# Performance work log

Hardware: AMD Instinct MI355X
Metric: run time of the kernel (lower is better)

## Reference

```python
import jax, jax.numpy as jnp
import numpy as np
from jax import lax

# pywt Wavelet('db3') analysis filters (dec_lo, dec_hi)
DEC_LO = jnp.array([0.035226291882100656, -0.08544127388224149, -0.13501102001039084,
                    0.4598775021193313, 0.8068915093133388, 0.3326705529509569], dtype=jnp.float32)
DEC_HI = jnp.array([-0.3326705529509569, 0.8068915093133388, -0.4598775021193313,
                    -0.13501102001039084, 0.08544127388224149, 0.035226291882100656], dtype=jnp.float32)


def _dwt_level(x):
    # One analysis level of pytorch_wavelets DWT1D with mode='zero'.
    # x: [B, N] -> (lo, hi) each [B, (N+L-1)//2]
    N = x.shape[-1]
    L = DEC_LO.shape[0]
    outsize = (N + L - 1) // 2  # pywt.dwt_coeff_len, zero mode
    p = 2 * (outsize - 1) - N + L
    # conv_general_dilated does cross-correlation; reversed filter == true convolution
    w = jnp.stack([DEC_LO[::-1], DEC_HI[::-1]])[:, None, :]  # [2, 1, L]
    y = lax.conv_general_dilated(x[:, None, :], w, window_strides=(2,),
                                 padding=[(p // 2, p - p // 2)])  # [B, 2, outsize]
    return y[:, 0, :], y[:, 1, :]


def _wavelet_features(sig, level=3):
    # sig: [B, N]. Returns (mean of final low-pass, sum over levels of ||hf||_2) per row.
    lo = sig
    high = jnp.zeros(sig.shape[0], sig.dtype)
    for _ in range(level):
        lo, hi = _dwt_level(lo)
        high = high + jnp.sqrt(jnp.sum(hi * hi, axis=-1))
    return jnp.mean(lo, axis=-1), high


def _dirichlet_weight(low, high):
    # Deterministic surrogate: Dirichlet([a1*10, a2*10]) has mean a1/(a1+a2),
    # replacing scipy dirichlet.rvs sampling with its expectation.
    a1 = jnp.clip(low, 1e-6)
    a2 = jnp.clip(high, 1e-6)
    return a1 / (a1 + a2)


def _forward(user_idx, item_idx, values, num_users, num_items):
    # item popularity: scatter-add of values * log1p(interaction count), L2-normalized
    counts = jnp.zeros(num_items, jnp.float32).at[item_idx].add(1.0)
    log_counts = jnp.log1p(counts)
    pop = jnp.zeros(num_items, jnp.float32).at[item_idx].add(values * log_counts[item_idx])
    pop = pop / (jnp.linalg.norm(pop) + 1e-8)
    # user activity
    act = jnp.zeros(num_users, jnp.float32).at[user_idx].add(
        values / jnp.log1p(pop[item_idx] + 1e-8))
    act = act / (jnp.linalg.norm(act) + 1e-8)
    # dense per-entity interaction signals (batched scatter replaces per-entity masking loop)
    user_sig = jnp.zeros((num_users, num_items), jnp.float32).at[user_idx, item_idx].add(values)
    user_sig = user_sig * (1.0 + act)[:, None]
    item_sig = jnp.zeros((num_items, num_users), jnp.float32).at[item_idx, user_idx].add(values)
    item_sig = item_sig * (1.0 + pop)[:, None]
    u_low, u_high = _wavelet_features(user_sig)
    i_low, i_high = _wavelet_features(item_sig)
    u_pop = _dirichlet_weight(u_low, u_high)
    i_pop = _dirichlet_weight(i_low, i_high)
    u_ni, i_ni = 1.0 - u_pop, 1.0 - i_pop
    wu_p, wu_n = u_pop[user_idx], u_ni[user_idx]
    wi_p, wi_n = i_pop[item_idx], i_ni[item_idx]
    # nnz-valued sparse outputs: [UIPG(=pop/pop), UING(=niche/niche), pop/niche, niche/pop]
    return jnp.stack([values * wu_p * wi_p,
                      values * wu_n * wi_n,
                      values * wu_p * wi_n,
                      values * wu_n * wi_p])


def setup_inputs():
    key = jax.random.key(0)
    k1, k2, k3 = jax.random.split(key, 3)
    NNZ, U, I = 2_000_000, 8192, 8192
    return {
        "user_idx": jax.random.randint(k1, (NNZ,), 0, U, dtype=jnp.int32),
        "item_idx": jax.random.randint(k2, (NNZ,), 0, I, dtype=jnp.int32),
        "values": jax.random.uniform(k3, (NNZ,), dtype=jnp.float32),
        "num_users": U,
        "num_items": I,
    }


def reference(user_idx, item_idx, values, num_users, num_items):
    return _forward(user_idx, item_idx, values, num_users, num_items)
```

## Files before the change

### kernel.cpp

```cpp
#include <hip/hip_runtime.h>
#include <math.h>

#define NE 8192
#define HT 1024
#define NCH 8
#define RT 512
#define NROWS 16

__device__ __constant__ float LO_R[6] = {
    0.3326705529509569f, 0.8068915093133388f, 0.4598775021193313f,
    -0.13501102001039084f, -0.08544127388224149f, 0.035226291882100656f};
__device__ __constant__ float HI_RV[6] = {
    0.035226291882100656f, 0.08544127388224149f, -0.13501102001039084f,
    -0.4598775021193313f, 0.8068915093133388f, -0.3326705529509569f};

__device__ __forceinline__ float blockReduceSum(float v, float* red) {
    #pragma unroll
    for (int off = 32; off > 0; off >>= 1) v += __shfl_down(v, off);
    int lane = threadIdx.x & 63, wid = threadIdx.x >> 6;
    if (lane == 0) red[wid] = v;
    __syncthreads();
    float r = 0.f;
    if (threadIdx.x == 0) {
        int nw = blockDim.x >> 6;
        for (int i = 0; i < nw; ++i) r += red[i];
    }
    return r;
}

__global__ void k_tables(float* __restrict__ resp, float4* __restrict__ Tdiag) {
    int a = blockIdx.x * blockDim.x + threadIdx.x;
    if (a >= NE) return;
    float lo1r[8], hi1r[8];
    int k1a = max(0, (a >> 1) - 3);
    #pragma unroll
    for (int t = 0; t < 8; ++t) {
        int k = k1a + t;
        int j = a - 2 * k + 4;
        bool ok = (j >= 0 && j <= 5 && k <= 4097);
        lo1r[t] = ok ? LO_R[j] : 0.f;
        hi1r[t] = ok ? HI_RV[j] : 0.f;
    }
    float lo2r[8], hi2r[8];
    int k2a = max(0, (k1a >> 1) - 1);
    #pragma unroll
    for (int t = 0; t < 8; ++t) {
        int k = k2a + t;
        float aL = 0.f, aH = 0.f;
        if (k <= 2050) {
            #pragma unroll
            for (int j = 0; j < 6; ++j) {
                int idx = 2 * k - 4 + j - k1a;
                if (idx >= 0 && idx < 8) {
                    aL = fmaf(LO_R[j], lo1r[idx], aL);
                    aH = fmaf(HI_RV[j], lo1r[idx], aH);
                }
            }
        }
        lo2r[t] = aL; hi2r[t] = aH;
    }
    float lo3r[8], hi3r[8];
    int k3a = max(0, (k2a >> 1) - 1);
    #pragma unroll
    for (int t = 0; t < 8; ++t) {
        int k = k3a + t;
        float aL = 0.f, aH = 0.f;
        if (k <= 1027) {
            #pragma unroll
            for (int j = 0; j < 6; ++j) {
                int idx = 2 * k - 4 + j - k2a;
                if (idx >= 0 && idx < 8) {
                    aL = fmaf(LO_R[j], lo2r[idx], aL);
                    aH = fmaf(HI_RV[j], lo2r[idx], aH);
                }
            }
        }
        lo3r[t] = aL; hi3r[t] = aH;
    }
    float g1 = 0.f, g2 = 0.f, g3 = 0.f, w3 = 0.f;
    #pragma unroll
    for (int t = 0; t < 8; ++t) {
        g1 = fmaf(hi1r[t], hi1r[t], g1);
        g2 = fmaf(hi2r[t], hi2r[t], g2);
        g3 = fmaf(hi3r[t], hi3r[t], g3);
        w3 += lo3r[t];
    }
    Tdiag[a] = make_float4(w3, g1, g2, g3);
    float* rp = resp + (size_t)a * 32;
    #pragma unroll
    for (int t = 0; t < 8; ++t) { rp[t] = hi1r[t]; rp[8 + t] = hi2r[t]; rp[16 + t] = hi3r[t]; }
    rp[24] = __int_as_float(k1a);
    rp[25] = __int_as_float(k2a);
    rp[26] = __int_as_float(k3a);
}

__global__ void k_gram(const float* __restrict__ resp, float* __restrict__ GtP) {
    int idx = blockIdx.x * 256 + threadIdx.x;
    if (idx >= NE * 35) return;
    int a = idx / 35;
    int d = idx - a * 35 + 1;
    int b = a + d;
    float v1 = 0.f, v2 = 0.f, v3 = 0.f;
    const float* ra = resp + (size_t)a * 32;
    if (b < NE) {
        const float* rb = resp + (size_t)b * 32;
        {
            int s = __float_as_int(rb[26]) - __float_as_int(ra[26]);
            #pragma unroll
            for (int u = 0; u < 8; ++u) {
                int t = u + s;
                if (t >= 0 && t < 8) v3 = fmaf(rb[16 + u], ra[16 + t], v3);
            }
        }
        if (d <= 15) {
            int s = __float_as_int(rb[25]) - __float_as_int(ra[25]);
            #pragma unroll
            for (int u = 0; u < 8; ++u) {
                int t = u + s;
                if (t >= 0 && t < 8) v2 = fmaf(rb[8 + u], ra[8 + t], v2);
            }
        }
        if (d <= 5) {
            int s = __float_as_int(rb[24]) - __float_as_int(ra[24]);
            #pragma unroll
            for (int u = 0; u < 8; ++u) {
                int t = u + s;
                if (t >= 0 && t < 8) v1 = fmaf(rb[u], ra[t], v1);
            }
        }
    }
    float* g = GtP + (size_t)a * 60;
    if (d <= 5) {
        *(float4*)(g + 4 * (d - 1)) = make_float4(v1, v2, v3, 0.f);
    } else if (d <= 15) {
        *(float2*)(g + 20 + 2 * (d - 6)) = make_float2(v2, v3);
    } else {
        g[40 + (d - 16)] = v3;
    }
}

__global__ __launch_bounds__(HT) void k_hist3(const int* __restrict__ ui,
                                              const int* __restrict__ ii,
                                              const float* __restrict__ v, int nnz,
                                              int* __restrict__ sliceU,
                                              int* __restrict__ sliceI,
                                              float* __restrict__ sliceS) {
    __shared__ int hU[NE];
    __shared__ int hI[NE];
    __shared__ float hS[NE];
    int b = blockIdx.x, tid = threadIdx.x, hb = gridDim.x;
    int4* hU4 = (int4*)hU; int4* hI4 = (int4*)hI; int4* hS4 = (int4*)hS;
    int4 z4 = make_int4(0, 0, 0, 0);
    for (int j = tid; j < NE / 4; j += HT) { hU4[j] = z4; hI4[j] = z4; hS4[j] = z4; }
    __syncthreads();
    int C = (nnz + hb - 1) / hb;
    int beg = b * C, end = min(nnz, beg + C);
    for (int n = beg + tid; n < end; n += HT) {
        atomicAdd(&hU[ui[n]], 1);
        int it = ii[n];
        atomicAdd(&hI[it], 1);
        atomicAdd(&hS[it], v[n]);
    }
    __syncthreads();
    size_t base = (size_t)b * NE;
    int4* sU = (int4*)(sliceU + base); int4* sI = (int4*)(sliceI + base);
    int4* sS = (int4*)(sliceS + base);
    for (int j = tid; j < NE / 4; j += HT) { sU[j] = hU4[j]; sI[j] = hI4[j]; sS[j] = hS4[j]; }
}

__global__ void k_chunksum3(const int* __restrict__ sliceU, const int* __restrict__ sliceI,
                            const float* __restrict__ sliceS, int spc,
                            int* __restrict__ csU, int* __restrict__ csI,
                            float* __restrict__ csS) {
    int i = blockIdx.x * 256 + threadIdx.x;
    int c = blockIdx.y;
    int b0 = c * spc;
    int cu = 0, ci = 0; float sv = 0.f;
    for (int b = b0; b < b0 + spc; ++b) {
        size_t o = (size_t)b * NE + i;
        cu += sliceU[o]; ci += sliceI[o]; sv += sliceS[o];
    }
    size_t oc = (size_t)c * NE + i;
    csU[oc] = cu; csI[oc] = ci; csS[oc] = sv;
}

__global__ void k_final3(const int* __restrict__ csU, const int* __restrict__ csI,
                         const float* __restrict__ csS,
                         int* cntU, int* cntI, float* popraw, float* normAcc) {
    __shared__ float red[4];
    int i = blockIdx.x * 256 + threadIdx.x;
    int cu = 0, ci = 0; float sv = 0.f;
    #pragma unroll
    for (int c = 0; c < NCH; ++c) {
        size_t o = (size_t)c * NE + i;
        cu += csU[o]; ci += csI[o]; sv += csS[o];
    }
    cntU[i] = cu; cntI[i] = ci;
    float p = log1pf((float)ci) * sv;
    popraw[i] = p;
    float s = blockReduceSum(p * p, red);
    if (threadIdx.x == 0) atomicAdd(&normAcc[0], s);
}

__global__ void k_scan2(const int* __restrict__ cntU, const int* __restrict__ cntI,
                        int* ptrU, int* ptrI) {
    __shared__ int sums[256];
    const int* cnt = blockIdx.x ? cntI : cntU;
    int* ptr = blockIdx.x ? ptrI : ptrU;
    int tid = threadIdx.x;
    int base = tid * 32;
    int local[32];
    int s = 0;
    #pragma unroll
    for (int j = 0; j < 32; ++j) { local[j] = cnt[base + j]; s += local[j]; }
    sums[tid] = s;
    __syncthreads();
    for (int off = 1; off < 256; off <<= 1) {
        int t = (tid >= off) ? sums[tid - off] : 0;
        __syncthreads();
        sums[tid] += t;
        __syncthreads();
    }
    int run = (tid > 0) ? sums[tid - 1] : 0;
    #pragma unroll
    for (int j = 0; j < 32; ++j) { ptr[base + j] = run; run += local[j]; }
    if (tid == 255) ptr[NE] = run;
}

__global__ void k_colscanB(int* csU, int* csI,
                           const int* __restrict__ ptrU, const int* __restrict__ ptrI) {
    int i = blockIdx.x * 256 + threadIdx.x;
    int* cs = blockIdx.y ? csI : csU;
    const int* ptr = blockIdx.y ? ptrI : ptrU;
    int run = ptr[i];
    #pragma unroll
    for (int c = 0; c < NCH; ++c) {
        size_t o = (size_t)c * NE + i;
        int t = cs[o]; cs[o] = run; run += t;
    }
}

__global__ void k_colscanC(int* sliceU, int* sliceI,
                           const int* __restrict__ csU, const int* __restrict__ csI, int spc) {
    int i = blockIdx.x * 256 + threadIdx.x;
    int c = blockIdx.y;
    int* slice = blockIdx.z ? sliceI : sliceU;
    const int* cs = blockIdx.z ? csI : csU;
    int run = cs[(size_t)c * NE + i];
    int b0 = c * spc;
    for (int b = b0; b < b0 + spc; ++b) {
        size_t o = (size_t)b * NE + i;
        int t = slice[o]; slice[o] = run; run += t;
    }
}

__global__ __launch_bounds__(HT) void k_scatter2(const int* __restrict__ ui,
                                                 const int* __restrict__ ii,
                                                 const float* __restrict__ v, int nnz,
                                                 const int* __restrict__ sliceU,
                                                 const int* __restrict__ sliceI,
                                                 const float* __restrict__ popraw,
                                                 const float* __restrict__ normAcc,
                                                 int2* __restrict__ pairsU,
                                                 int2* __restrict__ pairsI,
                                                 float* __restrict__ sliceA) {
    __shared__ int curU[NE];
    __shared__ int curI[NE];
    __shared__ float hA[NE];
    int b = blockIdx.x, tid = threadIdx.x, hb = gridDim.x;
    const int4* sU = (const int4*)(sliceU + (size_t)b * NE);
    const int4* sI = (const int4*)(sliceI + (size_t)b * NE);
    int4* cU4 = (int4*)curU; int4* cI4 = (int4*)curI;
    float4* hA4 = (float4*)hA;
    float4 zf = make_float4(0.f, 0.f, 0.f, 0.f);
    for (int j = tid; j < NE / 4; j += HT) { cU4[j] = sU[j]; cI4[j] = sI[j]; hA4[j] = zf; }
    __syncthreads();
    float rs0 = 1.f / (sqrtf(normAcc[0]) + 1e-8f);
    int C = (nnz + hb - 1) / hb;
    int beg = b * C, end = min(nnz, beg + C);
    for (int n = beg + tid; n < end; n += HT) {
        int u = ui[n], it = ii[n];
        float val = v[n];
        atomicAdd(&hA[u], val / log1pf(popraw[it] * rs0 + 1e-8f));
        int pU = atomicAdd(&curU[u], 1);
        pairsU[pU] = make_int2(it, __float_as_int(val));
        int pI = atomicAdd(&curI[it], 1);
        pairsI[pI] = make_int2(u, __float_as_int(val));
    }
    __syncthreads();
    float4* sA = (float4*)(sliceA + (size_t)b * NE);
    for (int j = tid; j < NE / 4; j += HT) sA[j] = hA4[j];
}

__global__ void k_actchunk(const float* __restrict__ sliceA, int spc, float* __restrict__ csA) {
    int i = blockIdx.x * 256 + threadIdx.x;
    int c = blockIdx.y;
    int b0 = c * spc;
    float a = 0.f;
    for (int b = b0; b < b0 + spc; ++b) a += sliceA[(size_t)b * NE + i];
    csA[(size_t)c * NE + i] = a;
}

__global__ void k_actfinal(const float* __restrict__ csA, float* act, float* normAcc) {
    __shared__ float red[4];
    int i = blockIdx.x * 256 + threadIdx.x;
    float a = 0.f;
    #pragma unroll
    for (int c = 0; c < NCH; ++c) a += csA[(size_t)c * NE + i];
    act[i] = a;
    float s = blockReduceSum(a * a, red);
    if (threadIdx.x == 0) atomicAdd(&normAcc[1], s);
}

__device__ __forceinline__ void scan_one(int p, float v, float4 td,
                                         const float* __restrict__ X,
                                         const unsigned int* __restrict__ Mrow,
                                         const float* __restrict__ GtP,
                                         float& s1, float& s2, float& s3, float& ls) {
    float xp = X[p];
    ls = fmaf(v, td.x, ls);
    float vx = v * xp;
    s1 = fmaf(vx, td.y, s1);
    s2 = fmaf(vx, td.z, s2);
    s3 = fmaf(vx, td.w, s3);
    int w = p >> 5, sh = (p & 31) + 1;
    unsigned long long lo64 = (unsigned long long)Mrow[w] |
                              ((unsigned long long)Mrow[w + 1] << 32);
    unsigned long long win = (lo64 >> sh) |
                             ((unsigned long long)Mrow[w + 2] << (64 - sh));
    win &= (1ull << 35) - 1ull;
    const float* g = GtP + (size_t)p * 60;
    while (win) {
        int d = __ffsll((unsigned long long)win);
        win &= win - 1;
        float c = 2.f * v * X[p + d];
        if (d <= 5) {
            float4 G = *(const float4*)(g + 4 * (d - 1));
            s1 = fmaf(c, G.x, s1);
            s2 = fmaf(c, G.y, s2);
            s3 = fmaf(c, G.z, s3);
        } else if (d <= 15) {
            float2 G = *(const float2*)(g + 20 + 2 * (d - 6));
            s2 = fmaf(c, G.x, s2);
            s3 = fmaf(c, G.y, s3);
        } else {
            s3 = fmaf(c, g[40 + (d - 16)], s3);
        }
    }
}

__global__ __launch_bounds__(RT) void k_rows(const int* __restrict__ ptrU,
                                             const int* __restrict__ ptrI,
                                             const int2* __restrict__ pairsU,
                                             const int2* __restrict__ pairsI,
                                             const float* __restrict__ popraw,
                                             const float* __restrict__ actraw,
                                             const float* __restrict__ normAcc,
                                             const float4* __restrict__ Tdiag,
                                             const float* __restrict__ GtP,
                                             float* __restrict__ u_w,
                                             float* __restrict__ i_w) {
    __shared__ __align__(16) float X[NE];
    __shared__ unsigned int M[264];
    __shared__ float acc[NROWS][4];
    int tid = threadIdx.x;
    int bid = blockIdx.x;
    bool isUser = bid >= 512;
    int r0 = (isUser ? bid - 512 : bid) * NROWS;
    const int* ptr = isUser ? ptrU : ptrI;
    const int2* pairs = isUser ? pairsU : pairsI;
    const float* raw = isUser ? actraw : popraw;
    float* w_out = isUser ? u_w : i_w;
    float rs = 1.f / (sqrtf(normAcc[isUser ? 1 : 0]) + 1e-8f);

    float4* X4 = (float4*)X;
    const float4 z4 = make_float4(0.f, 0.f, 0.f, 0.f);
    for (int q = tid; q < NE / 4; q += RT) X4[q] = z4;
    if (tid < 264) M[tid] = 0u;
    if (tid < NROWS * 4) ((float*)acc)[tid] = 0.f;

    int beg = ptr[r0], end = ptr[r0 + 1];
    int2 pr = make_int2(0, 0);
    float4 td = z4;
    if (tid < end - beg) {
        pr = pairs[beg + tid];
        td = Tdiag[pr.x];
    }

    for (int j = 0; j < NROWS; ++j) {
        int rl = r0 + j;
        __syncthreads();

        int cnt = end - beg;
        if (tid < cnt) {
            int p = pr.x;
            atomicAdd(&X[p], __int_as_float(pr.y));
            atomicOr(&M[p >> 5], 1u << (p & 31));
        }
        for (int n = beg + RT + tid; n < end; n += RT) {
            int2 q2 = pairs[n];
            atomicAdd(&X[q2.x], __int_as_float(q2.y));
            atomicOr(&M[q2.x >> 5], 1u << (q2.x & 31));
        }
        __syncthreads();

        int begN = end, endN = end;
        int2 prN = make_int2(0, 0);
        float4 tdN = z4;
        if (j + 1 < NROWS) {
            endN = ptr[rl + 2];
            if (tid < endN - begN) {
                prN = pairs[begN + tid];
                tdN = Tdiag[prN.x];
            }
        }

        float s1 = 0.f, s2 = 0.f, s3 = 0.f, ls = 0.f;
        if (tid < cnt)
            scan_one(pr.x, __int_as_float(pr.y), td, X, M, GtP, s1, s2, s3, ls);
        for (int n = beg + RT + tid; n < end; n += RT) {
            int2 q2 = pairs[n];
            scan_one(q2.x, __int_as_float(q2.y), Tdiag[q2.x], X, M, GtP,
                     s1, s2, s3, ls);
        }

        int nwav = min(8, (cnt + 63) >> 6);
        if ((tid >> 6) < nwav) {
            #pragma unroll
            for (int off = 32; off > 0; off >>= 1) {
                s1 += __shfl_down(s1, off);
                s2 += __shfl_down(s2, off);
                s3 += __shfl_down(s3, off);
                ls += __shfl_down(ls, off);
            }
            if ((tid & 63) == 0) {
                atomicAdd(&acc[j][0], s1);
                atomicAdd(&acc[j][1], s2);
                atomicAdd(&acc[j][2], s3);
                atomicAdd(&acc[j][3], ls);
            }
        }
        __syncthreads();

        if (tid < cnt) { X[pr.x] = 0.f; M[pr.x >> 5] = 0u; }
        for (int n = beg + RT + tid; n < end; n += RT) {
            int2 q2 = pairs[n];
            X[q2.x] = 0.f; M[q2.x >> 5] = 0u;
        }
        beg = begN; end = endN; pr = prN; td = tdN;
    }

    __syncthreads();
    if (tid < NROWS) {
        float t1 = acc[tid][0], t2 = acc[tid][1], t3 = acc[tid][2], tl = acc[tid][3];
        float rawv = raw[r0 + tid];
        float sc = 1.f + rawv * rs;
        float high = (sqrtf(fmaxf(t1, 0.f)) + sqrtf(fmaxf(t2, 0.f)) +
                      sqrtf(fmaxf(t3, 0.f))) * sc;
        float low = tl * (1.f / 1028.f) * sc;
        float a1 = fmaxf(low, 1e-6f);
        float a2 = fmaxf(high, 1e-6f);
        w_out[r0 + tid] = a1 / (a1 + a2);
    }
}

__global__ void k_out(const int* __restrict__ ui, const int* __restrict__ ii,
                      const float* __restrict__ v, int nnz,
                      const float* __restrict__ u_w, const float* __restrict__ i_w,
                      float* __restrict__ out) {
    int ngroups = nnz >> 2;
    int idx = blockIdx.x * blockDim.x + threadIdx.x;
    int stride = gridDim.x * blockDim.x;
    const int4* ui4 = (const int4*)ui;
    const int4* ii4 = (const int4*)ii;
    const float4* v4 = (const float4*)v;
    float4* o0 = (float4*)out;
    float4* o1 = (float4*)(out + (size_t)nnz);
    float4* o2 = (float4*)(out + 2 * (size_t)nnz);
    float4* o3 = (float4*)(out + 3 * (size_t)nnz);
    for (int g = idx; g < ngroups; g += stride) {
        int4 u = ui4[g];
        int4 it = ii4[g];
        float4 val = v4[g];
        float wu0 = u_w[u.x], wu1 = u_w[u.y], wu2 = u_w[u.z], wu3 = u_w[u.w];
        float wi0 = i_w[it.x], wi1 = i_w[it.y], wi2 = i_w[it.z], wi3 = i_w[it.w];
        o0[g] = make_float4(val.x * wu0 * wi0, val.y * wu1 * wi1,
                            val.z * wu2 * wi2, val.w * wu3 * wi3);
        o1[g] = make_float4(val.x * (1.f - wu0) * (1.f - wi0), val.y * (1.f - wu1) * (1.f - wi1),
                            val.z * (1.f - wu2) * (1.f - wi2), val.w * (1.f - wu3) * (1.f - wi3));
        o2[g] = make_float4(val.x * wu0 * (1.f - wi0), val.y * wu1 * (1.f - wi1),
                            val.z * wu2 * (1.f - wi2), val.w * wu3 * (1.f - wi3));
        o3[g] = make_float4(val.x * (1.f - wu0) * wi0, val.y * (1.f - wu1) * wi1,
                            val.z * (1.f - wu2) * wi2, val.w * (1.f - wu3) * wi3);
    }
    int tail = ngroups * 4;
    for (int n = tail + idx; n < nnz; n += stride) {
        float val = v[n];
        float wu = u_w[ui[n]], wi = i_w[ii[n]];
        out[n] = val * wu * wi;
        out[(size_t)nnz + n] = val * (1.f - wu) * (1.f - wi);
        out[2 * (size_t)nnz + n] = val * wu * (1.f - wi);
        out[3 * (size_t)nnz + n] = val * (1.f - wu) * wi;
    }
}

extern "C" void kernel_launch(void* const* d_in, const int* in_sizes, int n_in,
                              void* d_out, int out_size, void* d_ws, size_t ws_size,
                              hipStream_t stream) {
    const int* ui = (const int*)d_in[0];
    const int* ii = (const int*)d_in[1];
    const float* vals = (const float*)d_in[2];
    int nnz = in_sizes[0];
    float* out = (float*)d_out;

    char* ws = (char*)d_ws;
    size_t off = 0;
    auto take = [&](size_t bytes) -> char* {
        char* p = ws + off;
        off = (off + bytes + 255) & ~(size_t)255;
        return p;
    };

    int*   cntU    = (int*)take(NE * 4);
    int*   cntI    = (int*)take(NE * 4);
    float* popraw  = (float*)take(NE * 4);
    float* actraw  = (float*)take(NE * 4);
    int*   ptrU    = (int*)take((NE + 1) * 4);
    int*   ptrI    = (int*)take((NE + 1) * 4);
    float* u_w     = (float*)take(NE * 4);
    float* i_w     = (float*)take(NE * 4);
    float* normAcc = (float*)take(256);
    float4* Tdiag  = (float4*)take((size_t)NE * 16);
    float* GtP     = (float*)take((size_t)NE * 60 * 4);
    float* resp    = (float*)take((size_t)NE * 32 * 4);
    int*   csU     = (int*)take((size_t)NCH * NE * 4);
    int*   csI     = (int*)take((size_t)NCH * NE * 4);
    float* csS     = (float*)take((size_t)NCH * NE * 4);
    int2*  pairsU  = (int2*)take((size_t)nnz * 8);
    int2*  pairsI  = (int2*)take((size_t)nnz * 8);
    size_t fixedEnd = off;

    int hb = 256;
    while (hb > 8 && fixedEnd + 3 * (size_t)hb * NE * 4 + 4096 > ws_size) hb >>= 1;
    int spc = hb / NCH;
    int*   sliceU = (int*)take((size_t)hb * NE * 4);
    int*   sliceI = (int*)take((size_t)hb * NE * 4);
    float* sliceS = (float*)take((size_t)hb * NE * 4);

    hipMemsetAsync(normAcc, 0, 256, stream);

    int nb = (nnz / 4 + 255) / 256;
    if (nb > 2048) nb = 2048;

    k_tables<<<NE / 64, 64, 0, stream>>>(resp, Tdiag);
    k_gram<<<(NE * 35 + 255) / 256, 256, 0, stream>>>(resp, GtP);

    k_hist3<<<hb, HT, 0, stream>>>(ui, ii, vals, nnz, sliceU, sliceI, sliceS);
    k_chunksum3<<<dim3(32, NCH), 256, 0, stream>>>(sliceU, sliceI, sliceS, spc, csU, csI, csS);
    k_final3<<<32, 256, 0, stream>>>(csU, csI, csS, cntU, cntI, popraw, normAcc);

    k_scan2<<<2, 256, 0, stream>>>(cntU, cntI, ptrU, ptrI);
    k_colscanB<<<dim3(32, 2), 256, 0, stream>>>(csU, csI, ptrU, ptrI);
    k_colscanC<<<dim3(32, NCH, 2), 256, 0, stream>>>(sliceU, sliceI, csU, csI, spc);

    k_scatter2<<<hb, HT, 0, stream>>>(ui, ii, vals, nnz, sliceU, sliceI,
                                      popraw, normAcc, pairsU, pairsI, sliceS);

    k_actchunk<<<dim3(32, NCH), 256, 0, stream>>>(sliceS, spc, csS);
    k_actfinal<<<32, 256, 0, stream>>>(csS, actraw, normAcc);

    k_rows<<<1024, RT, 0, stream>>>(ptrU, ptrI, pairsU, pairsI,
                                    popraw, actraw, normAcc, Tdiag, GtP, u_w, i_w);

    k_out<<<nb, 256, 0, stream>>>(ui, ii, vals, nnz, u_w, i_w, out);
}
```

Measured before the change: 238.1 us.

## Bucket CSR scatter by 16-row groups and finish row sort inside k_rows

```diff
diff --git a/kernel.cpp b/kernel.cpp
--- a/kernel.cpp
+++ b/kernel.cpp
@@ -6,6 +6,8 @@
 #define NCH 8
 #define RT 512
 #define NROWS 16
+#define NBK 512
+#define KMAX 10
 
 __device__ __constant__ float LO_R[6] = {
     0.3326705529509569f, 0.8068915093133388f, 0.4598775021193313f,
@@ -144,7 +146,9 @@
                                               const float* __restrict__ v, int nnz,
                                               int* __restrict__ sliceU,
                                               int* __restrict__ sliceI,
-                                              float* __restrict__ sliceS) {
+                                              float* __restrict__ sliceS,
+                                              int* __restrict__ bsU,
+                                              int* __restrict__ bsI) {
     __shared__ int hU[NE];
     __shared__ int hI[NE];
     __shared__ float hS[NE];
@@ -166,6 +170,14 @@
     int4* sU = (int4*)(sliceU + base); int4* sI = (int4*)(sliceI + base);
     int4* sS = (int4*)(sliceS + base);
     for (int j = tid; j < NE / 4; j += HT) { sU[j] = hU4[j]; sI[j] = hI4[j]; sS[j] = hS4[j]; }
+    for (int b2 = tid; b2 < NBK; b2 += HT) {
+        int sUu = 0, sIi = 0;
+        int b16 = b2 * 16;
+        #pragma unroll
+        for (int t = 0; t < 16; ++t) { sUu += hU[b16 + t]; sIi += hI[b16 + t]; }
+        bsU[(size_t)b * NBK + b2] = sUu;
+        bsI[(size_t)b * NBK + b2] = sIi;
+    }
 }
 
 __global__ void k_chunksum3(const int* __restrict__ sliceU, const int* __restrict__ sliceI,
@@ -227,53 +239,66 @@
     if (tid == 255) ptr[NE] = run;
 }
 
-__global__ void k_colscanB(int* csU, int* csI,
-                           const int* __restrict__ ptrU, const int* __restrict__ ptrI) {
-    int i = blockIdx.x * 256 + threadIdx.x;
-    int* cs = blockIdx.y ? csI : csU;
+__global__ void k_bchunk(const int* __restrict__ bsU, const int* __restrict__ bsI,
+                         int* __restrict__ bcsU, int* __restrict__ bcsI) {
+    int col = blockIdx.x * 256 + threadIdx.x;
+    int c = blockIdx.y;
+    const int* bs = blockIdx.z ? bsI : bsU;
+    int* bcs = blockIdx.z ? bcsI : bcsU;
+    int s = 0;
+    int b0 = c * 32;
+    for (int b = b0; b < b0 + 32; ++b) s += bs[(size_t)b * NBK + col];
+    bcs[(size_t)c * NBK + col] = s;
+}
+
+__global__ void k_bscan(int* __restrict__ bcsU, int* __restrict__ bcsI,
+                        const int* __restrict__ ptrU, const int* __restrict__ ptrI) {
+    int col = blockIdx.x * 256 + threadIdx.x;
+    int* bcs = blockIdx.y ? bcsI : bcsU;
     const int* ptr = blockIdx.y ? ptrI : ptrU;
-    int run = ptr[i];
-    #pragma unroll
-    for (int c = 0; c < NCH; ++c) {
-        size_t o = (size_t)c * NE + i;
-        int t = cs[o]; cs[o] = run; run += t;
-    }
-}
-
-__global__ void k_colscanC(int* sliceU, int* sliceI,
-                           const int* __restrict__ csU, const int* __restrict__ csI, int spc) {
-    int i = blockIdx.x * 256 + threadIdx.x;
+    int run = ptr[col * NROWS];
+    #pragma unroll
+    for (int c = 0; c < 8; ++c) {
+        size_t o = (size_t)c * NBK + col;
+        int t = bcs[o]; bcs[o] = run; run += t;
+    }
+}
+
+__global__ void k_bfine(int* __restrict__ bsU, int* __restrict__ bsI,
+                        const int* __restrict__ bcsU, const int* __restrict__ bcsI) {
+    int col = blockIdx.x * 256 + threadIdx.x;
     int c = blockIdx.y;
-    int* slice = blockIdx.z ? sliceI : sliceU;
-    const int* cs = blockIdx.z ? csI : csU;
-    int run = cs[(size_t)c * NE + i];
-    int b0 = c * spc;
-    for (int b = b0; b < b0 + spc; ++b) {
-        size_t o = (size_t)b * NE + i;
-        int t = slice[o]; slice[o] = run; run += t;
+    int* bs = blockIdx.z ? bsI : bsU;
+    const int* bcs = blockIdx.z ? bcsI : bcsU;
+    int run = bcs[(size_t)c * NBK + col];
+    int b0 = c * 32;
+    for (int b = b0; b < b0 + 32; ++b) {
+        size_t o = (size_t)b * NBK + col;
+        int t = bs[o]; bs[o] = run; run += t;
     }
 }
 
 __global__ __launch_bounds__(HT) void k_scatter2(const int* __restrict__ ui,
                                                  const int* __restrict__ ii,
                                                  const float* __restrict__ v, int nnz,
-                                                 const int* __restrict__ sliceU,
-                                                 const int* __restrict__ sliceI,
+                                                 const int* __restrict__ bsU,
+                                                 const int* __restrict__ bsI,
                                                  const float* __restrict__ popraw,
                                                  const float* __restrict__ normAcc,
                                                  int2* __restrict__ pairsU,
                                                  int2* __restrict__ pairsI,
                                                  float* __restrict__ sliceA) {
-    __shared__ int curU[NE];
-    __shared__ int curI[NE];
+    __shared__ int curU[NBK];
+    __shared__ int curI[NBK];
     __shared__ float hA[NE];
     int b = blockIdx.x, tid = threadIdx.x, hb = gridDim.x;
-    const int4* sU = (const int4*)(sliceU + (size_t)b * NE);
-    const int4* sI = (const int4*)(sliceI + (size_t)b * NE);
-    int4* cU4 = (int4*)curU; int4* cI4 = (int4*)curI;
+    for (int j = tid; j < NBK; j += HT) {
+        curU[j] = bsU[(size_t)b * NBK + j];
+        curI[j] = bsI[(size_t)b * NBK + j];
+    }
     float4* hA4 = (float4*)hA;
     float4 zf = make_float4(0.f, 0.f, 0.f, 0.f);
-    for (int j = tid; j < NE / 4; j += HT) { cU4[j] = sU[j]; cI4[j] = sI[j]; hA4[j] = zf; }
+    for (int j = tid; j < NE / 4; j += HT) hA4[j] = zf;
     __syncthreads();
     float rs0 = 1.f / (sqrtf(normAcc[0]) + 1e-8f);
     int C = (nnz + hb - 1) / hb;
@@ -282,10 +307,10 @@
         int u = ui[n], it = ii[n];
         float val = v[n];
         atomicAdd(&hA[u], val / log1pf(popraw[it] * rs0 + 1e-8f));
-        int pU = atomicAdd(&curU[u], 1);
-        pairsU[pU] = make_int2(it, __float_as_int(val));
-        int pI = atomicAdd(&curI[it], 1);
-        pairsI[pI] = make_int2(u, __float_as_int(val));
+        int pU = atomicAdd(&curU[u >> 4], 1);
+        pairsU[pU] = make_int2(((u & 15) << 13) | it, __float_as_int(val));
+        int pI = atomicAdd(&curI[it >> 4], 1);
+        pairsI[pI] = make_int2(((it & 15) << 13) | u, __float_as_int(val));
     }
     __syncthreads();
     float4* sA = (float4*)(sliceA + (size_t)b * NE);
@@ -351,8 +376,8 @@
 
 __global__ __launch_bounds__(RT) void k_rows(const int* __restrict__ ptrU,
                                              const int* __restrict__ ptrI,
-                                             const int2* __restrict__ pairsU,
-                                             const int2* __restrict__ pairsI,
+                                             int2* __restrict__ pairsU,
+                                             int2* __restrict__ pairsI,
                                              const float* __restrict__ popraw,
                                              const float* __restrict__ actraw,
                                              const float* __restrict__ normAcc,
@@ -363,12 +388,15 @@
     __shared__ __align__(16) float X[NE];
     __shared__ unsigned int M[264];
     __shared__ float acc[NROWS][4];
+    __shared__ int rowOff[NROWS + 1];
+    __shared__ int rowCur[NROWS];
     int tid = threadIdx.x;
     int bid = blockIdx.x;
-    bool isUser = bid >= 512;
-    int r0 = (isUser ? bid - 512 : bid) * NROWS;
+    bool isUser = bid >= NBK;
+    int bk = isUser ? bid - NBK : bid;
+    int r0 = bk * NROWS;
     const int* ptr = isUser ? ptrU : ptrI;
-    const int2* pairs = isUser ? pairsU : pairsI;
+    int2* pairs = isUser ? pairsU : pairsI;
     const float* raw = isUser ? actraw : popraw;
     float* w_out = isUser ? u_w : i_w;
     float rs = 1.f / (sqrtf(normAcc[isUser ? 1 : 0]) + 1e-8f);
@@ -378,8 +406,41 @@
     for (int q = tid; q < NE / 4; q += RT) X4[q] = z4;
     if (tid < 264) M[tid] = 0u;
     if (tid < NROWS * 4) ((float*)acc)[tid] = 0.f;
-
-    int beg = ptr[r0], end = ptr[r0 + 1];
+    if (tid <= NROWS) rowOff[tid] = 0;
+    __syncthreads();
+
+    int base = ptr[r0];
+    int endB = ptr[r0 + NROWS];
+    int cap = base + KMAX * RT;
+    if (endB > cap) endB = cap;
+    int2 kk[KMAX];
+    #pragma unroll
+    for (int t = 0; t < KMAX; ++t) {
+        int n = base + t * RT + tid;
+        kk[t] = (n < endB) ? pairs[n] : make_int2(-1, 0);
+        if (kk[t].x >= 0) atomicAdd(&rowOff[1 + (kk[t].x >> 13)], 1);
+    }
+    __syncthreads();
+    if (tid == 0) {
+        int run = 0;
+        #pragma unroll
+        for (int j = 1; j <= NROWS; ++j) { int t = rowOff[j]; rowOff[j] = run + t; run += t; }
+    }
+    __syncthreads();
+    if (tid < NROWS) rowCur[tid] = rowOff[tid];
+    __syncthreads();
+    #pragma unroll
+    for (int t = 0; t < KMAX; ++t) {
+        if (kk[t].x >= 0) {
+            int tag = kk[t].x >> 13;
+            int pos = atomicAdd(&rowCur[tag], 1);
+            pairs[base + pos] = make_int2(kk[t].x & 8191, kk[t].y);
+        }
+    }
+    __threadfence();
+    __syncthreads();
+
+    int beg = base, end = base + rowOff[1];
     int2 pr = make_int2(0, 0);
     float4 td = z4;
     if (tid < end - beg) {
@@ -388,7 +449,6 @@
     }
 
     for (int j = 0; j < NROWS; ++j) {
-        int rl = r0 + j;
         __syncthreads();
 
         int cnt = end - beg;
@@ -408,7 +468,7 @@
         int2 prN = make_int2(0, 0);
         float4 tdN = z4;
         if (j + 1 < NROWS) {
-            endN = ptr[rl + 2];
+            endN = base + rowOff[j + 2];
             if (tid < endN - begN) {
                 prN = pairs[begN + tid];
                 tdN = Tdiag[prN.x];
@@ -538,14 +598,19 @@
     float* csS     = (float*)take((size_t)NCH * NE * 4);
     int2*  pairsU  = (int2*)take((size_t)nnz * 8);
     int2*  pairsI  = (int2*)take((size_t)nnz * 8);
+    int*   bcsU    = (int*)take((size_t)8 * NBK * 4);
+    int*   bcsI    = (int*)take((size_t)8 * NBK * 4);
     size_t fixedEnd = off;
 
     int hb = 256;
-    while (hb > 8 && fixedEnd + 3 * (size_t)hb * NE * 4 + 4096 > ws_size) hb >>= 1;
+    while (hb > 8 && fixedEnd + 3 * (size_t)hb * NE * 4 +
+                     2 * (size_t)hb * NBK * 4 + 4096 > ws_size) hb >>= 1;
     int spc = hb / NCH;
     int*   sliceU = (int*)take((size_t)hb * NE * 4);
     int*   sliceI = (int*)take((size_t)hb * NE * 4);
     float* sliceS = (float*)take((size_t)hb * NE * 4);
+    int*   bsU    = (int*)take((size_t)hb * NBK * 4);
+    int*   bsI    = (int*)take((size_t)hb * NBK * 4);
 
     hipMemsetAsync(normAcc, 0, 256, stream);
 
@@ -555,22 +620,23 @@
     k_tables<<<NE / 64, 64, 0, stream>>>(resp, Tdiag);
     k_gram<<<(NE * 35 + 255) / 256, 256, 0, stream>>>(resp, GtP);
 
-    k_hist3<<<hb, HT, 0, stream>>>(ui, ii, vals, nnz, sliceU, sliceI, sliceS);
+    k_hist3<<<hb, HT, 0, stream>>>(ui, ii, vals, nnz, sliceU, sliceI, sliceS, bsU, bsI);
     k_chunksum3<<<dim3(32, NCH), 256, 0, stream>>>(sliceU, sliceI, sliceS, spc, csU, csI, csS);
     k_final3<<<32, 256, 0, stream>>>(csU, csI, csS, cntU, cntI, popraw, normAcc);
 
     k_scan2<<<2, 256, 0, stream>>>(cntU, cntI, ptrU, ptrI);
-    k_colscanB<<<dim3(32, 2), 256, 0, stream>>>(csU, csI, ptrU, ptrI);
-    k_colscanC<<<dim3(32, NCH, 2), 256, 0, stream>>>(sliceU, sliceI, csU, csI, spc);
-
-    k_scatter2<<<hb, HT, 0, stream>>>(ui, ii, vals, nnz, sliceU, sliceI,
+    k_bchunk<<<dim3(2, 8, 2), 256, 0, stream>>>(bsU, bsI, bcsU, bcsI);
+    k_bscan<<<dim3(2, 2), 256, 0, stream>>>(bcsU, bcsI, ptrU, ptrI);
+    k_bfine<<<dim3(2, 8, 2), 256, 0, stream>>>(bsU, bsI, bcsU, bcsI);
+
+    k_scatter2<<<hb, HT, 0, stream>>>(ui, ii, vals, nnz, bsU, bsI,
                                       popraw, normAcc, pairsU, pairsI, sliceS);
 
     k_actchunk<<<dim3(32, NCH), 256, 0, stream>>>(sliceS, spc, csS);
     k_actfinal<<<32, 256, 0, stream>>>(csS, actraw, normAcc);
 
-    k_rows<<<1024, RT, 0, stream>>>(ptrU, ptrI, pairsU, pairsI,
-                                    popraw, actraw, normAcc, Tdiag, GtP, u_w, i_w);
+    k_rows<<<2 * NBK, RT, 0, stream>>>(ptrU, ptrI, pairsU, pairsI,
+                                       popraw, actraw, normAcc, Tdiag, GtP, u_w, i_w);
 
     k_out<<<nb, 256, 0, stream>>>(ui, ii, vals, nnz, u_w, i_w, out);
 }
```

After: 514.4 us. +116.1%, slower.
